# Kernel optimization log

Measured on AMD Instinct MI355X. Metric: run time of the kernel, lower is better.

Reference implementation:

```python
import jax, jax.numpy as jnp
import numpy as np

N_NODES = 100000
N_EDGES = 1600000
IN_DIM, HID_DIM, OUT_DIM = 128, 64, 64
NEG_SLOPE = 0.2


def _gat_layer(h_in, src, dst, W, a_src, a_dst, b, n_nodes):
    # h: [N, F_out]
    h = h_in @ W.T
    alpha_src = h @ a_src  # [N]
    alpha_dst = h @ a_dst  # [N]
    # per-edge raw attention logits (edge j->i: src=j, dst=i)
    e = jax.nn.leaky_relu(alpha_src[src] + alpha_dst[dst], NEG_SLOPE)  # [E]
    # segment softmax over incoming edges of each dst node
    m = jax.ops.segment_max(e, dst, num_segments=n_nodes)
    ex = jnp.exp(e - m[dst])
    denom = jax.ops.segment_sum(ex, dst, num_segments=n_nodes)
    alpha = ex / denom[dst]  # [E], denom > 0 thanks to self-loops
    out = jax.ops.segment_sum(h[src] * alpha[:, None], dst, num_segments=n_nodes)
    return out + b


def setup_inputs() -> dict:
    key = jax.random.key(0)
    ks = jax.random.split(key, 12)
    x = jax.random.normal(ks[0], (N_NODES, IN_DIM), dtype=jnp.float32)
    edge_index = jax.random.randint(ks[1], (2, N_EDGES), 0, N_NODES)
    edge_attr = jax.random.normal(ks[2], (N_EDGES, 1), dtype=jnp.float32)
    s1 = 1.0 / np.sqrt(IN_DIM)
    s2 = 1.0 / np.sqrt(HID_DIM)
    W1 = jax.random.normal(ks[3], (HID_DIM, IN_DIM), dtype=jnp.float32) * s1
    att_src1 = jax.random.normal(ks[4], (HID_DIM,), dtype=jnp.float32) * s2
    att_dst1 = jax.random.normal(ks[5], (HID_DIM,), dtype=jnp.float32) * s2
    b1 = jnp.zeros((HID_DIM,), dtype=jnp.float32)
    W2 = jax.random.normal(ks[6], (OUT_DIM, HID_DIM), dtype=jnp.float32) * s2
    att_src2 = jax.random.normal(ks[7], (OUT_DIM,), dtype=jnp.float32) * s2
    att_dst2 = jax.random.normal(ks[8], (OUT_DIM,), dtype=jnp.float32) * s2
    b2 = jnp.zeros((OUT_DIM,), dtype=jnp.float32)
    return {"x": x, "edge_index": edge_index, "edge_attr": edge_attr,
            "W1": W1, "att_src1": att_src1, "att_dst1": att_dst1, "b1": b1,
            "W2": W2, "att_src2": att_src2, "att_dst2": att_dst2, "b2": b2}


def reference(x, edge_index, edge_attr, W1, att_src1, att_dst1, b1,
              W2, att_src2, att_dst2, b2):
    n = x.shape[0]
    # add self-loops (PyG GATConv default); edge_attr unused (edge_dim=None)
    loop = jnp.arange(n, dtype=edge_index.dtype)
    src = jnp.concatenate([edge_index[0], loop])
    dst = jnp.concatenate([edge_index[1], loop])
    h = _gat_layer(x, src, dst, W1, att_src1, att_dst1, b1, n)
    h = jax.nn.relu(h)
    h = _gat_layer(h, src, dst, W2, att_src2, att_dst2, b2, n)
    # global_mean_pool with batch=None -> mean over all nodes, shape [1, F]
    return jnp.mean(h, axis=0, keepdims=True)
```

## Files before the change

### kernel.cpp

```cpp
#include <hip/hip_runtime.h>

#define NEG_SLOPE 0.2f
#define BSHIFT 6
#define NBMAX 2048
#define BCAP 1408
#define CHUNK 4096

typedef __attribute__((ext_vector_type(8))) short short8;
typedef __attribute__((ext_vector_type(4))) float f32x4;

__device__ __forceinline__ unsigned short f2b(float x) {
    unsigned u = __float_as_uint(x);
    u += 0x7fff + ((u >> 16) & 1);
    return (unsigned short)(u >> 16);
}
__device__ __forceinline__ float b2f(unsigned short u) {
    return __uint_as_float((unsigned)u << 16);
}

__global__ __launch_bounds__(256) void hist_kernel(
    const int* __restrict__ ei, int* __restrict__ hist, int E, int NB)
{
    __shared__ int cnt[NBMAX];
    const int tid = threadIdx.x;
    for (int i = tid; i < NB; i += 256) cnt[i] = 0;
    __syncthreads();
    const int start = blockIdx.x * CHUNK;
    const int end = min(start + CHUNK, E);
    for (int i = start + tid; i < end; i += 256)
        atomicAdd(&cnt[ei[E + i] >> BSHIFT], 1);
    __syncthreads();
    for (int i = tid; i < NB; i += 256)
        hist[(size_t)blockIdx.x * NB + i] = cnt[i];
}

__global__ __launch_bounds__(256) void colscan_kernel(
    int* __restrict__ hist, int* __restrict__ btotal, int NB, int NBLK)
{
    const int col = (int)((blockIdx.x * 256 + threadIdx.x) >> 6);
    const int ln  = threadIdx.x & 63;
    if (col >= NB) return;
    int run = 0;
    for (int r0 = 0; r0 < NBLK; r0 += 64) {
        const int r = r0 + ln;
        const bool ok = (r < NBLK);
        int v = ok ? hist[(size_t)r * NB + col] : 0;
        int inc = v;
        #pragma unroll
        for (int off = 1; off < 64; off <<= 1) {
            int x = __shfl_up(inc, off, 64);
            if (ln >= off) inc += x;
        }
        if (ok) hist[(size_t)r * NB + col] = run + inc - v;
        run += __shfl(inc, 63, 64);
    }
    if (ln == 0) btotal[col] = run;
}

__global__ __launch_bounds__(256) void scatter_kernel(
    const int* __restrict__ ei, const int* __restrict__ hist,
    int* __restrict__ binned, int E, int NB)
{
    __shared__ int base[NBMAX], cnt2[NBMAX];
    const int nblk = gridDim.x;
    const int q = nblk >> 3, rr = nblk & 7;
    const int x = blockIdx.x & 7, k = blockIdx.x >> 3;
    const int chunk = ((x < rr) ? x * (q + 1) : rr * (q + 1) + (x - rr) * q) + k;

    const int tid = threadIdx.x;
    for (int i = tid; i < NB; i += 256) {
        base[i] = hist[(size_t)chunk * NB + i];
        cnt2[i] = 0;
    }
    __syncthreads();
    const int start = chunk * CHUNK;
    const int end = min(start + CHUNK, E);
    for (int i = start + tid; i < end; i += 256) {
        int s = ei[i], d = ei[E + i];
        int b = d >> BSHIFT;
        int r = base[b] + atomicAdd(&cnt2[b], 1);
        if (r < BCAP) binned[(size_t)b * BCAP + r] = (s << BSHIFT) | (d & 63);
    }
}

__global__ __launch_bounds__(256) void bscan_kernel(
    const int* __restrict__ btotal, int* __restrict__ bbase, int NB)
{
    __shared__ int lds[256];
    const int t = threadIdx.x;
    int v[8]; int s = 0;
    #pragma unroll
    for (int j = 0; j < 8; ++j) {
        int i = t * 8 + j;
        v[j] = (i < NB) ? min(btotal[i], BCAP) : 0;
        s += v[j];
    }
    lds[t] = s;
    __syncthreads();
    #pragma unroll
    for (int off = 1; off < 256; off <<= 1) {
        int x = (t >= off) ? lds[t - off] : 0;
        __syncthreads();
        lds[t] += x;
        __syncthreads();
    }
    int excl = (t > 0) ? lds[t - 1] : 0;
    #pragma unroll
    for (int j = 0; j < 8; ++j) {
        int i = t * 8 + j;
        if (i < NB) { bbase[i] = excl + 64 * i; excl += v[j]; }
    }
}

__global__ __launch_bounds__(256) void bucket_csr_kernel(
    const int* __restrict__ binned, const int* __restrict__ btotal,
    const int* __restrict__ bbase, int* __restrict__ row_ptr,
    int* __restrict__ esrc, int N)
{
    __shared__ int ldeg[64];
    __shared__ int lcur[64];
    const int b = blockIdx.x;
    const int tid = threadIdx.x;
    const int node0 = b << BSHIFT;
    const int cnt = min(btotal[b], BCAP);
    const int base_e = bbase[b];
    const int* bp = binned + (size_t)b * BCAP;

    if (tid < 64) ldeg[tid] = (node0 + tid < N) ? 1 : 0;
    __syncthreads();
    for (int i = tid; i < cnt; i += 256)
        atomicAdd(&ldeg[bp[i] & 63], 1);
    __syncthreads();
    if (tid < 64) {
        int v = ldeg[tid];
        int inc = v;
        #pragma unroll
        for (int off = 1; off < 64; off <<= 1) {
            int t2 = __shfl_up(inc, off, 64);
            if (tid >= off) inc += t2;
        }
        int excl = inc - v;
        int node = node0 + tid;
        if (node <= N) row_ptr[node] = base_e + excl;
        if (node < N) {
            esrc[base_e + excl] = node;
            lcur[tid] = base_e + excl + 1;
        }
    }
    __syncthreads();
    for (int i = tid; i < cnt; i += 256) {
        int v = bp[i];
        int pos = atomicAdd(&lcur[v & 63], 1);
        esrc[pos] = v >> BSHIFT;
    }
}

template<int K, bool BF16IN>
__global__ __launch_bounds__(256) void gemm_attn_kernel(
    const void* __restrict__ in_v, const float* __restrict__ W,
    const float* __restrict__ a_src, const float* __restrict__ a_dst,
    unsigned short* __restrict__ hb, float* __restrict__ asrc,
    float* __restrict__ adst, int N)
{
    constexpr int LDK = K + 8;
    __shared__ unsigned short xb[64 * LDK];
    __shared__ unsigned short wb[64 * LDK];
    __shared__ float avs[64], avd[64];

    const int tid = threadIdx.x;
    const int node0 = blockIdx.x * 64;
    const int w = tid >> 6;
    const int lane = tid & 63;
    const int col = lane & 15;
    const int quad = lane >> 4;

    if (tid < 64) { avs[tid] = a_src[tid]; avd[tid] = a_dst[tid]; }

    for (int i = tid; i < 64 * (K / 4); i += 256) {
        int r = i / (K / 4), c = i % (K / 4);
        float4 v = *(const float4*)&W[(size_t)r * K + 4 * c];
        *(ushort4*)&wb[r * LDK + 4 * c] =
            make_ushort4(f2b(v.x), f2b(v.y), f2b(v.z), f2b(v.w));
    }
    if (BF16IN) {
        const unsigned short* in = (const unsigned short*)in_v;
        for (int i = tid; i < 64 * (K / 8); i += 256) {
            int r = i / (K / 8), c = i % (K / 8);
            int node = node0 + r;
            ulonglong2 v = (node < N)
                ? *(const ulonglong2*)&in[(size_t)node * K + 8 * c]
                : make_ulonglong2(0ull, 0ull);
            *(ulonglong2*)&xb[r * LDK + 8 * c] = v;
        }
    } else {
        const float* in = (const float*)in_v;
        for (int i = tid; i < 64 * (K / 4); i += 256) {
            int r = i / (K / 4), c = i % (K / 4);
            int node = node0 + r;
            float4 v = (node < N) ? *(const float4*)&in[(size_t)node * K + 4 * c]
                                  : make_float4(0.f, 0.f, 0.f, 0.f);
            *(ushort4*)&xb[r * LDK + 4 * c] =
                make_ushort4(f2b(v.x), f2b(v.y), f2b(v.z), f2b(v.w));
        }
    }
    __syncthreads();

    f32x4 acc[4] = {f32x4{0,0,0,0}, f32x4{0,0,0,0}, f32x4{0,0,0,0}, f32x4{0,0,0,0}};
    #pragma unroll
    for (int kc = 0; kc < K / 32; ++kc) {
        short8 a = *(const short8*)&xb[(16 * w + col) * LDK + kc * 32 + quad * 8];
        #pragma unroll
        for (int j = 0; j < 4; ++j) {
            short8 b = *(const short8*)&wb[(16 * j + col) * LDK + kc * 32 + quad * 8];
            acc[j] = __builtin_amdgcn_mfma_f32_16x16x32_bf16(a, b, acc[j], 0, 0, 0);
        }
    }

    #pragma unroll
    for (int r = 0; r < 4; ++r) {
        const int node = node0 + 16 * w + quad * 4 + r;
        const bool valid = node < N;
        float vs = 0.f, vd = 0.f;
        #pragma unroll
        for (int j = 0; j < 4; ++j) {
            float hv = acc[j][r];
            int f = 16 * j + col;
            if (valid) hb[(size_t)node * 64 + f] = f2b(hv);
            vs = fmaf(hv, avs[f], vs);
            vd = fmaf(hv, avd[f], vd);
        }
        #pragma unroll
        for (int off = 8; off >= 1; off >>= 1) {
            vs += __shfl_down(vs, off, 16);
            vd += __shfl_down(vd, off, 16);
        }
        if (col == 0 && valid) { asrc[node] = vs; adst[node] = vd; }
    }
}

__global__ __launch_bounds__(256) void aggregate_csr_kernel(
    const int* __restrict__ row_ptr, const int* __restrict__ esrc,
    const float* __restrict__ asrc, const float* __restrict__ adst,
    const unsigned short* __restrict__ hb, const float* __restrict__ bias,
    unsigned short* __restrict__ gb, int N, int do_relu)
{
    const int node = (int)((blockIdx.x * 256 + threadIdx.x) >> 4);
    const int lane = threadIdx.x & 15;
    if (node >= N) return;
    const int beg = row_ptr[node];
    const int end = row_ptr[node + 1];
    const float ad = adst[node];
    float a0 = 0.f, a1 = 0.f, a2 = 0.f, a3 = 0.f, wsum = 0.f;
    int p = beg;
    for (; p + 8 <= end; p += 8) {
        int s[8]; ushort4 r[8]; float l[8];
        #pragma unroll
        for (int j = 0; j < 8; ++j) s[j] = esrc[p + j];
        #pragma unroll
        for (int j = 0; j < 8; ++j)
            r[j] = *(const ushort4*)(hb + (size_t)s[j] * 64 + lane * 4);
        #pragma unroll
        for (int j = 0; j < 8; ++j) l[j] = asrc[s[j]] + ad;
        #pragma unroll
        for (int j = 0; j < 8; ++j) {
            float ll = (l[j] > 0.f) ? l[j] : NEG_SLOPE * l[j];
            float w = __expf(ll);
            wsum += w;
            a0 = fmaf(w, b2f(r[j].x), a0);
            a1 = fmaf(w, b2f(r[j].y), a1);
            a2 = fmaf(w, b2f(r[j].z), a2);
            a3 = fmaf(w, b2f(r[j].w), a3);
        }
    }
    for (; p < end; ++p) {
        int s = esrc[p];
        ushort4 r = *(const ushort4*)(hb + (size_t)s * 64 + lane * 4);
        float l = asrc[s] + ad;
        l = (l > 0.f) ? l : NEG_SLOPE * l;
        float w = __expf(l);
        wsum += w;
        a0 = fmaf(w, b2f(r.x), a0);
        a1 = fmaf(w, b2f(r.y), a1);
        a2 = fmaf(w, b2f(r.z), a2);
        a3 = fmaf(w, b2f(r.w), a3);
    }
    const float inv = 1.0f / wsum;
    float4 v = make_float4(a0 * inv, a1 * inv, a2 * inv, a3 * inv);
    if (bias) {
        v.x += bias[lane * 4 + 0]; v.y += bias[lane * 4 + 1];
        v.z += bias[lane * 4 + 2]; v.w += bias[lane * 4 + 3];
    }
    if (do_relu) {
        v.x = fmaxf(v.x, 0.f); v.y = fmaxf(v.y, 0.f);
        v.z = fmaxf(v.z, 0.f); v.w = fmaxf(v.w, 0.f);
    }
    *(ushort4*)&gb[(size_t)node * 64 + lane * 4] =
        make_ushort4(f2b(v.x), f2b(v.y), f2b(v.z), f2b(v.w));
}

__global__ __launch_bounds__(256) void pool_kernel(
    const unsigned short* __restrict__ gb, const float* __restrict__ b2,
    float* __restrict__ out, int N)
{
    __shared__ float red[256];
    const int f = threadIdx.x & 63;
    const int sub = threadIdx.x >> 6;
    float acc = 0.f;
    for (int n = blockIdx.x * 4 + sub; n < N; n += gridDim.x * 4)
        acc += b2f(gb[(size_t)n * 64 + f]);
    red[threadIdx.x] = acc;
    __syncthreads();
    if (threadIdx.x < 64) {
        float s = red[f] + red[64 + f] + red[128 + f] + red[192 + f];
        atomicAdd(out + f, s * (1.0f / (float)N));
        if (blockIdx.x == 0) atomicAdd(out + f, b2[f]);
    }
}

extern "C" void kernel_launch(void* const* d_in, const int* in_sizes, int n_in,
                              void* d_out, int out_size, void* d_ws, size_t ws_size,
                              hipStream_t stream) {
    const float* x   = (const float*)d_in[0];
    const int*   ei  = (const int*)d_in[1];
    const float* W1  = (const float*)d_in[3];
    const float* as1 = (const float*)d_in[4];
    const float* ad1 = (const float*)d_in[5];
    const float* b1  = (const float*)d_in[6];
    const float* W2  = (const float*)d_in[7];
    const float* as2 = (const float*)d_in[8];
    const float* ad2 = (const float*)d_in[9];
    const float* b2  = (const float*)d_in[10];
    float* out = (float*)d_out;

    const int N = in_sizes[0] / 128;
    const int E = in_sizes[1] / 2;
    const int Etot = E + N;
    const int NB = (N + 63) >> BSHIFT;
    const int NBLK = (E + CHUNK - 1) / CHUNK;

    auto align4 = [](size_t v) { return (v + 3) & ~(size_t)3; };
    float* ws    = (float*)d_ws;
    size_t off = 0;
    unsigned short* hb = (unsigned short*)(ws + off); off += align4((size_t)N * 32);
    unsigned short* gb = (unsigned short*)(ws + off); off += align4((size_t)N * 32);
    float* asrc  = ws + off; off += align4(N);
    float* adst  = ws + off; off += align4(N);
    int* row_ptr = (int*)(ws + off); off += align4(N + 1);
    int* btotal  = (int*)(ws + off); off += NBMAX;
    int* bbase   = (int*)(ws + off); off += NBMAX;
    int* hist    = (int*)(ws + off); off += align4((size_t)NBLK * NB);
    int* esrc    = (int*)(ws + off); off += align4(Etot);
    int* binned  = (int*)gb;

    const int gemm_blocks = (N + 63) / 64;
    const int agg_blocks  = (int)(((size_t)N * 16 + 255) / 256);

    hipMemsetAsync(out, 0, 64 * sizeof(float), stream);

    hist_kernel<<<NBLK, 256, 0, stream>>>(ei, hist, E, NB);
    colscan_kernel<<<(NB * 64 + 255) / 256, 256, 0, stream>>>(hist, btotal, NB, NBLK);
    scatter_kernel<<<NBLK, 256, 0, stream>>>(ei, hist, binned, E, NB);
    bscan_kernel<<<1, 256, 0, stream>>>(btotal, bbase, NB);
    bucket_csr_kernel<<<NB, 256, 0, stream>>>(binned, btotal, bbase, row_ptr, esrc, N);

    gemm_attn_kernel<128, false><<<gemm_blocks, 256, 0, stream>>>(
        x, W1, as1, ad1, hb, asrc, adst, N);
    aggregate_csr_kernel<<<agg_blocks, 256, 0, stream>>>(
        row_ptr, esrc, asrc, adst, hb, b1, gb, N, 1);

    gemm_attn_kernel<64, true><<<gemm_blocks, 256, 0, stream>>>(
        gb, W2, as2, ad2, hb, asrc, adst, N);
    aggregate_csr_kernel<<<agg_blocks, 256, 0, stream>>>(
        row_ptr, esrc, asrc, adst, hb, nullptr, gb, N, 0);

    pool_kernel<<<512, 256, 0, stream>>>(gb, b2, out, N);
}
```

Before: 289.0 us.

## Fuse edge scatter with layer-1 GEMM and drop bucket prefix scan

Measured after the change: 271.1 us. 6.2% less time.

```diff
diff --git a/kernel.cpp b/kernel.cpp
--- a/kernel.cpp
+++ b/kernel.cpp
@@ -4,6 +4,7 @@
 #define BSHIFT 6
 #define NBMAX 2048
 #define BCAP 1408
+#define ESTRIDE (BCAP + 64)
 #define CHUNK 4096
 
 typedef __attribute__((ext_vector_type(8))) short short8;
@@ -57,118 +58,18 @@
     if (ln == 0) btotal[col] = run;
 }
 
-__global__ __launch_bounds__(256) void scatter_kernel(
-    const int* __restrict__ ei, const int* __restrict__ hist,
-    int* __restrict__ binned, int E, int NB)
-{
-    __shared__ int base[NBMAX], cnt2[NBMAX];
-    const int nblk = gridDim.x;
-    const int q = nblk >> 3, rr = nblk & 7;
-    const int x = blockIdx.x & 7, k = blockIdx.x >> 3;
-    const int chunk = ((x < rr) ? x * (q + 1) : rr * (q + 1) + (x - rr) * q) + k;
-
-    const int tid = threadIdx.x;
-    for (int i = tid; i < NB; i += 256) {
-        base[i] = hist[(size_t)chunk * NB + i];
-        cnt2[i] = 0;
-    }
-    __syncthreads();
-    const int start = chunk * CHUNK;
-    const int end = min(start + CHUNK, E);
-    for (int i = start + tid; i < end; i += 256) {
-        int s = ei[i], d = ei[E + i];
-        int b = d >> BSHIFT;
-        int r = base[b] + atomicAdd(&cnt2[b], 1);
-        if (r < BCAP) binned[(size_t)b * BCAP + r] = (s << BSHIFT) | (d & 63);
-    }
-}
-
-__global__ __launch_bounds__(256) void bscan_kernel(
-    const int* __restrict__ btotal, int* __restrict__ bbase, int NB)
-{
-    __shared__ int lds[256];
-    const int t = threadIdx.x;
-    int v[8]; int s = 0;
-    #pragma unroll
-    for (int j = 0; j < 8; ++j) {
-        int i = t * 8 + j;
-        v[j] = (i < NB) ? min(btotal[i], BCAP) : 0;
-        s += v[j];
-    }
-    lds[t] = s;
-    __syncthreads();
-    #pragma unroll
-    for (int off = 1; off < 256; off <<= 1) {
-        int x = (t >= off) ? lds[t - off] : 0;
-        __syncthreads();
-        lds[t] += x;
-        __syncthreads();
-    }
-    int excl = (t > 0) ? lds[t - 1] : 0;
-    #pragma unroll
-    for (int j = 0; j < 8; ++j) {
-        int i = t * 8 + j;
-        if (i < NB) { bbase[i] = excl + 64 * i; excl += v[j]; }
-    }
-}
-
-__global__ __launch_bounds__(256) void bucket_csr_kernel(
-    const int* __restrict__ binned, const int* __restrict__ btotal,
-    const int* __restrict__ bbase, int* __restrict__ row_ptr,
-    int* __restrict__ esrc, int N)
-{
-    __shared__ int ldeg[64];
-    __shared__ int lcur[64];
-    const int b = blockIdx.x;
-    const int tid = threadIdx.x;
-    const int node0 = b << BSHIFT;
-    const int cnt = min(btotal[b], BCAP);
-    const int base_e = bbase[b];
-    const int* bp = binned + (size_t)b * BCAP;
-
-    if (tid < 64) ldeg[tid] = (node0 + tid < N) ? 1 : 0;
-    __syncthreads();
-    for (int i = tid; i < cnt; i += 256)
-        atomicAdd(&ldeg[bp[i] & 63], 1);
-    __syncthreads();
-    if (tid < 64) {
-        int v = ldeg[tid];
-        int inc = v;
-        #pragma unroll
-        for (int off = 1; off < 64; off <<= 1) {
-            int t2 = __shfl_up(inc, off, 64);
-            if (tid >= off) inc += t2;
-        }
-        int excl = inc - v;
-        int node = node0 + tid;
-        if (node <= N) row_ptr[node] = base_e + excl;
-        if (node < N) {
-            esrc[base_e + excl] = node;
-            lcur[tid] = base_e + excl + 1;
-        }
-    }
-    __syncthreads();
-    for (int i = tid; i < cnt; i += 256) {
-        int v = bp[i];
-        int pos = atomicAdd(&lcur[v & 63], 1);
-        esrc[pos] = v >> BSHIFT;
-    }
-}
-
 template<int K, bool BF16IN>
-__global__ __launch_bounds__(256) void gemm_attn_kernel(
+__device__ __forceinline__ void gemm_attn_core(
+    unsigned short* __restrict__ xb, unsigned short* __restrict__ wb,
+    float* __restrict__ avs, float* __restrict__ avd, int bid,
     const void* __restrict__ in_v, const float* __restrict__ W,
     const float* __restrict__ a_src, const float* __restrict__ a_dst,
     unsigned short* __restrict__ hb, float* __restrict__ asrc,
     float* __restrict__ adst, int N)
 {
     constexpr int LDK = K + 8;
-    __shared__ unsigned short xb[64 * LDK];
-    __shared__ unsigned short wb[64 * LDK];
-    __shared__ float avs[64], avd[64];
-
     const int tid = threadIdx.x;
-    const int node0 = blockIdx.x * 64;
+    const int node0 = bid * 64;
     const int w = tid >> 6;
     const int lane = tid & 63;
     const int col = lane & 15;
@@ -238,8 +139,108 @@
     }
 }
 
+__global__ __launch_bounds__(256) void scatter_gemm_kernel(
+    const int* __restrict__ ei, const int* __restrict__ hist,
+    int* __restrict__ binned, int E, int NB, int nblk,
+    const float* __restrict__ x, const float* __restrict__ W1,
+    const float* __restrict__ as1, const float* __restrict__ ad1,
+    unsigned short* __restrict__ hb, float* __restrict__ asrc,
+    float* __restrict__ adst, int N)
+{
+    extern __shared__ char smem[];
+    if ((int)blockIdx.x < nblk) {
+        int* base = (int*)smem;
+        int* cnt2 = base + NBMAX;
+        const int q = nblk >> 3, rr = nblk & 7;
+        const int xs = blockIdx.x & 7, k = blockIdx.x >> 3;
+        const int chunk = ((xs < rr) ? xs * (q + 1) : rr * (q + 1) + (xs - rr) * q) + k;
+        const int tid = threadIdx.x;
+        for (int i = tid; i < NB; i += 256) {
+            base[i] = hist[(size_t)chunk * NB + i];
+            cnt2[i] = 0;
+        }
+        __syncthreads();
+        const int start = chunk * CHUNK;
+        const int end = min(start + CHUNK, E);
+        for (int i = start + tid; i < end; i += 256) {
+            int s = ei[i], d = ei[E + i];
+            int b = d >> BSHIFT;
+            int r = base[b] + atomicAdd(&cnt2[b], 1);
+            if (r < BCAP) binned[(size_t)b * BCAP + r] = (s << BSHIFT) | (d & 63);
+        }
+    } else {
+        constexpr int LDK = 128 + 8;
+        unsigned short* xb = (unsigned short*)smem;
+        unsigned short* wb = xb + 64 * LDK;
+        float* avs = (float*)(wb + 64 * LDK);
+        float* avd = avs + 64;
+        gemm_attn_core<128, false>(xb, wb, avs, avd, (int)blockIdx.x - nblk,
+                                   x, W1, as1, ad1, hb, asrc, adst, N);
+    }
+}
+
+__global__ __launch_bounds__(256) void bucket_csr_kernel(
+    const int* __restrict__ binned, const int* __restrict__ btotal,
+    int* __restrict__ row_ptr, int* __restrict__ rend,
+    int* __restrict__ esrc, int N)
+{
+    __shared__ int ldeg[64];
+    __shared__ int lcur[64];
+    const int b = blockIdx.x;
+    const int tid = threadIdx.x;
+    const int node0 = b << BSHIFT;
+    const int cnt = min(btotal[b], BCAP);
+    const int base_e = b * ESTRIDE;
+    const int* bp = binned + (size_t)b * BCAP;
+
+    if (tid < 64) ldeg[tid] = (node0 + tid < N) ? 1 : 0;
+    __syncthreads();
+    for (int i = tid; i < cnt; i += 256)
+        atomicAdd(&ldeg[bp[i] & 63], 1);
+    __syncthreads();
+    if (tid < 64) {
+        int v = ldeg[tid];
+        int inc = v;
+        #pragma unroll
+        for (int off = 1; off < 64; off <<= 1) {
+            int t2 = __shfl_up(inc, off, 64);
+            if (tid >= off) inc += t2;
+        }
+        int excl = inc - v;
+        int node = node0 + tid;
+        if (node < N) {
+            row_ptr[node] = base_e + excl;
+            rend[node] = base_e + excl + v;
+            esrc[base_e + excl] = node;
+            lcur[tid] = base_e + excl + 1;
+        }
+    }
+    __syncthreads();
+    for (int i = tid; i < cnt; i += 256) {
+        int v = bp[i];
+        int pos = atomicAdd(&lcur[v & 63], 1);
+        esrc[pos] = v >> BSHIFT;
+    }
+}
+
+template<int K, bool BF16IN>
+__global__ __launch_bounds__(256) void gemm_attn_kernel(
+    const void* __restrict__ in_v, const float* __restrict__ W,
+    const float* __restrict__ a_src, const float* __restrict__ a_dst,
+    unsigned short* __restrict__ hb, float* __restrict__ asrc,
+    float* __restrict__ adst, int N)
+{
+    constexpr int LDK = K + 8;
+    __shared__ unsigned short xb[64 * LDK];
+    __shared__ unsigned short wb[64 * LDK];
+    __shared__ float avs[64], avd[64];
+    gemm_attn_core<K, BF16IN>(xb, wb, avs, avd, (int)blockIdx.x,
+                              in_v, W, a_src, a_dst, hb, asrc, adst, N);
+}
+
 __global__ __launch_bounds__(256) void aggregate_csr_kernel(
-    const int* __restrict__ row_ptr, const int* __restrict__ esrc,
+    const int* __restrict__ row_ptr, const int* __restrict__ rend,
+    const int* __restrict__ esrc,
     const float* __restrict__ asrc, const float* __restrict__ adst,
     const unsigned short* __restrict__ hb, const float* __restrict__ bias,
     unsigned short* __restrict__ gb, int N, int do_relu)
@@ -248,21 +249,21 @@
     const int lane = threadIdx.x & 15;
     if (node >= N) return;
     const int beg = row_ptr[node];
-    const int end = row_ptr[node + 1];
+    const int end = rend[node];
     const float ad = adst[node];
     float a0 = 0.f, a1 = 0.f, a2 = 0.f, a3 = 0.f, wsum = 0.f;
     int p = beg;
-    for (; p + 8 <= end; p += 8) {
-        int s[8]; ushort4 r[8]; float l[8];
-        #pragma unroll
-        for (int j = 0; j < 8; ++j) s[j] = esrc[p + j];
-        #pragma unroll
-        for (int j = 0; j < 8; ++j)
+    for (; p + 4 <= end; p += 4) {
+        int s[4]; ushort4 r[4]; float l[4];
+        #pragma unroll
+        for (int j = 0; j < 4; ++j) s[j] = esrc[p + j];
+        #pragma unroll
+        for (int j = 0; j < 4; ++j)
             r[j] = *(const ushort4*)(hb + (size_t)s[j] * 64 + lane * 4);
         #pragma unroll
-        for (int j = 0; j < 8; ++j) l[j] = asrc[s[j]] + ad;
-        #pragma unroll
-        for (int j = 0; j < 8; ++j) {
+        for (int j = 0; j < 4; ++j) l[j] = asrc[s[j]] + ad;
+        #pragma unroll
+        for (int j = 0; j < 4; ++j) {
             float ll = (l[j] > 0.f) ? l[j] : NEG_SLOPE * l[j];
             float w = __expf(ll);
             wsum += w;
@@ -334,7 +335,6 @@
 
     const int N = in_sizes[0] / 128;
     const int E = in_sizes[1] / 2;
-    const int Etot = E + N;
     const int NB = (N + 63) >> BSHIFT;
     const int NBLK = (E + CHUNK - 1) / CHUNK;
 
@@ -345,33 +345,32 @@
     unsigned short* gb = (unsigned short*)(ws + off); off += align4((size_t)N * 32);
     float* asrc  = ws + off; off += align4(N);
     float* adst  = ws + off; off += align4(N);
-    int* row_ptr = (int*)(ws + off); off += align4(N + 1);
+    int* row_ptr = (int*)(ws + off); off += align4(N);
+    int* rend    = (int*)(ws + off); off += align4(N);
     int* btotal  = (int*)(ws + off); off += NBMAX;
-    int* bbase   = (int*)(ws + off); off += NBMAX;
     int* hist    = (int*)(ws + off); off += align4((size_t)NBLK * NB);
-    int* esrc    = (int*)(ws + off); off += align4(Etot);
+    int* esrc    = (int*)(ws + off); off += align4((size_t)NB * ESTRIDE);
     int* binned  = (int*)gb;
 
     const int gemm_blocks = (N + 63) / 64;
     const int agg_blocks  = (int)(((size_t)N * 16 + 255) / 256);
+    const int packed_lds  = 64 * (128 + 8) * 2 * 2 + 2 * 64 * 4;
 
     hipMemsetAsync(out, 0, 64 * sizeof(float), stream);
 
     hist_kernel<<<NBLK, 256, 0, stream>>>(ei, hist, E, NB);
     colscan_kernel<<<(NB * 64 + 255) / 256, 256, 0, stream>>>(hist, btotal, NB, NBLK);
-    scatter_kernel<<<NBLK, 256, 0, stream>>>(ei, hist, binned, E, NB);
-    bscan_kernel<<<1, 256, 0, stream>>>(btotal, bbase, NB);
-    bucket_csr_kernel<<<NB, 256, 0, stream>>>(binned, btotal, bbase, row_ptr, esrc, N);
-
-    gemm_attn_kernel<128, false><<<gemm_blocks, 256, 0, stream>>>(
-        x, W1, as1, ad1, hb, asrc, adst, N);
+    scatter_gemm_kernel<<<NBLK + gemm_blocks, 256, packed_lds, stream>>>(
+        ei, hist, binned, E, NB, NBLK, x, W1, as1, ad1, hb, asrc, adst, N);
+    bucket_csr_kernel<<<NB, 256, 0, stream>>>(binned, btotal, row_ptr, rend, esrc, N);
+
     aggregate_csr_kernel<<<agg_blocks, 256, 0, stream>>>(
-        row_ptr, esrc, asrc, adst, hb, b1, gb, N, 1);
+        row_ptr, rend, esrc, asrc, adst, hb, b1, gb, N, 1);
 
     gemm_attn_kernel<64, true><<<gemm_blocks, 256, 0, stream>>>(
         gb, W2, as2, ad2, hb, asrc, adst, N);
     aggregate_csr_kernel<<<agg_blocks, 256, 0, stream>>>(
-        row_ptr, esrc, asrc, adst, hb, nullptr, gb, N, 0);
+        row_ptr, rend, esrc, asrc, adst, hb, nullptr, gb, N, 0);
 
     pool_kernel<<<512, 256, 0, stream>>>(gb, b2, out, N);
 }
```
